# Kernel tuning notes

Hardware: AMD Instinct MI355X
Metric: run time of the kernel (lower is better)

Reference implementation:

```python
import jax, jax.numpy as jnp
import numpy as np

N, SD, VD, LD = 8192, 512, 4096, 768
TAU = 0.5
K = 6    # topk over stru->mm similarity
K2 = 6   # topk2 over mm->mm similarity
BN_EPS = 1e-5
LRELU_SLOPE = 0.01


def _mlp_bn(x, W1, b1, W2, b2, gamma, beta):
    # Linear -> LeakyReLU -> Linear -> BatchNorm1d (training mode, batch stats)
    h = x @ W1 + b1
    h = jnp.where(h >= 0, h, LRELU_SLOPE * h)
    h = h @ W2 + b2
    mu = h.mean(axis=0)
    var = h.var(axis=0)  # biased variance, as torch BN uses for normalization
    return (h - mu) / jnp.sqrt(var + BN_EPS) * gamma + beta


def _cossim(x, y):
    xn = x / (jnp.linalg.norm(x, axis=-1, keepdims=True) + 1e-12)
    yn = y / (jnp.linalg.norm(y, axis=-1, keepdims=True) + 1e-12)
    return xn @ yn.T


def _neibor_mnce_v2(stru, mm):
    sm = jnp.exp(_cossim(stru, mm) / TAU)   # [N, N]
    mmd = _cossim(mm, mm)                    # [N, N]
    _, maxSM = jax.lax.top_k(sm, K)          # [N, K]
    rows = jnp.arange(stru.shape[0])[:, None]
    pos = []
    for i in range(K):  # fixed small loop over topk columns (as in original)
        idx = maxSM[:, i]                         # [N]
        _, mm_idx = jax.lax.top_k(mmd[idx], K2)   # gather rows then topk -> [N, K2]
        pos.append(sm[rows, mm_idx])              # [N, K2]
    pos = jnp.concatenate(pos, axis=-1)           # [N, K*K2]
    return jnp.mean(-jnp.log(pos.sum(-1) / sm.sum(-1)))


def setup_inputs() -> dict:
    key = jax.random.key(0)
    ks = jax.random.split(key, 11)
    d = {
        'stru_feats': jax.random.normal(ks[0], (N, SD), jnp.float32),
        'visu_feats': jax.random.normal(ks[1], (N, VD), jnp.float32),
        'ling_feats': jax.random.normal(ks[2], (N, LD), jnp.float32),
        # fusion_l_vl params
        'Wl1': jax.random.normal(ks[3], (LD, SD), jnp.float32) / np.sqrt(LD),
        'bl1': jnp.zeros((SD,), jnp.float32),
        'Wl2': jax.random.normal(ks[4], (SD, SD), jnp.float32) / np.sqrt(SD),
        'bl2': jnp.zeros((SD,), jnp.float32),
        'gl': jnp.ones((SD,), jnp.float32),
        'betal': jnp.zeros((SD,), jnp.float32),
        # fusion_v_vl params
        'Wv1': jax.random.normal(ks[5], (VD, SD), jnp.float32) / np.sqrt(VD),
        'bv1': jnp.zeros((SD,), jnp.float32),
        'Wv2': jax.random.normal(ks[6], (SD, SD), jnp.float32) / np.sqrt(SD),
        'bv2': jnp.zeros((SD,), jnp.float32),
        'gv': jnp.ones((SD,), jnp.float32),
        'betav': jnp.zeros((SD,), jnp.float32),
    }
    return d


def reference(stru_feats, visu_feats, ling_feats,
              Wl1, bl1, Wl2, bl2, gl, betal,
              Wv1, bv1, Wv2, bv2, gv, betav):
    ling = _mlp_bn(ling_feats, Wl1, bl1, Wl2, bl2, gl, betal)
    visu = _mlp_bn(visu_feats, Wv1, bv1, Wv2, bv2, gv, betav)
    loss_sl = _neibor_mnce_v2(stru_feats, ling)
    loss_sv = _neibor_mnce_v2(stru_feats, visu)
    return (loss_sl + loss_sv, ling, visu)
```

## Files before the change

kernel.cpp:

```cpp
#include <hip/hip_runtime.h>
#include <hip/hip_bf16.h>
#include <math.h>

typedef __bf16 bf16;
typedef __attribute__((ext_vector_type(8))) __bf16 bf16x8;
typedef __attribute__((ext_vector_type(4))) float floatx4;

static_assert(sizeof(bf16x8) == 16, "bf16x8 must be 16B");

__global__ void row_normalize_kernel(const float* __restrict__ x, bf16* __restrict__ out) {
  __shared__ float red[256];
  int row = blockIdx.x;
  int t = threadIdx.x;
  float v0 = x[(size_t)row * 512 + t];
  float v1 = x[(size_t)row * 512 + t + 256];
  red[t] = v0 * v0 + v1 * v1;
  __syncthreads();
  for (int d = 128; d > 0; d >>= 1) {
    if (t < d) red[t] += red[t + d];
    __syncthreads();
  }
  float scale = 1.0f / (sqrtf(red[0]) + 1e-12f);
  out[(size_t)row * 512 + t] = (bf16)(v0 * scale);
  out[(size_t)row * 512 + t + 256] = (bf16)(v1 * scale);
}

__global__ void transpose_cast_kernel(const float* __restrict__ W, bf16* __restrict__ Wt, int K) {
  int k0 = blockIdx.x * 64;
  int n0 = blockIdx.y * 64;
  for (int i = threadIdx.x; i < 64 * 64; i += 256) {
    int kk = i & 63, nn = i >> 6;
    Wt[(size_t)(n0 + nn) * K + (k0 + kk)] = (bf16)W[(size_t)(k0 + kk) * 512 + (n0 + nn)];
  }
}

__global__ void bn_stats_kernel(const float* __restrict__ h, float* __restrict__ colsum,
                                float* __restrict__ colsumsq) {
  int col = threadIdx.x;
  int r0 = blockIdx.x * 32;
  float s = 0.f, s2 = 0.f;
  for (int r = r0; r < r0 + 32; ++r) {
    float v = h[(size_t)r * 512 + col];
    s += v;
    s2 += v * v;
  }
  atomicAdd(&colsum[col], s);
  atomicAdd(&colsumsq[col], s2);
}

__global__ void bn_apply_kernel(const float* __restrict__ h, const float* __restrict__ colsum,
                                const float* __restrict__ colsumsq, const float* __restrict__ gamma,
                                const float* __restrict__ beta, float* __restrict__ mm_out,
                                bf16* __restrict__ mmn) {
  __shared__ float red[512];
  int row = blockIdx.x, col = threadIdx.x;
  float mean = colsum[col] * (1.0f / 8192.0f);
  float var = colsumsq[col] * (1.0f / 8192.0f) - mean * mean;
  float inv = rsqrtf(var + 1e-5f);
  float y = (h[(size_t)row * 512 + col] - mean) * inv * gamma[col] + beta[col];
  mm_out[(size_t)row * 512 + col] = y;
  red[col] = y * y;
  __syncthreads();
  for (int d = 256; d > 0; d >>= 1) {
    if (col < d) red[col] += red[col + d];
    __syncthreads();
  }
  float scale = 1.0f / (sqrtf(red[0]) + 1e-12f);
  mmn[(size_t)row * 512 + col] = (bf16)(y * scale);
}

template <int MODE, bool AF32>
__launch_bounds__(256, 2) __global__
void gemm_nt_kernel(const void* __restrict__ Av, const bf16* __restrict__ B,
                    const float* __restrict__ bias, bf16* __restrict__ out_bf,
                    float* __restrict__ out_f, int K) {
  __shared__ __align__(16) bf16 As[64][72];
  __shared__ __align__(16) bf16 Bs[64][72];

  const int tid = threadIdx.x;
  const int lane = tid & 63;
  const int wave = tid >> 6;
  const int q = lane >> 4;
  const int ml = lane & 15;
  const int row0 = blockIdx.x * 64;
  const int col0 = blockIdx.y * 64;

  const float* Af = (const float*)Av;
  const bf16* Ab = (const bf16*)Av;

  floatx4 acc[4];
#pragma unroll
  for (int f = 0; f < 4; ++f) acc[f] = (floatx4)0.0f;

  for (int kt = 0; kt < K; kt += 64) {
    __syncthreads();
    for (int i = tid; i < 512; i += 256) {
      int r = i >> 3, c = (i & 7) << 3;
      if constexpr (AF32) {
        const float* p = Af + (size_t)(row0 + r) * K + kt + c;
        bf16x8 v;
#pragma unroll
        for (int e = 0; e < 8; ++e) v[e] = (bf16)p[e];
        *(bf16x8*)&As[r][c] = v;
      } else {
        *(bf16x8*)&As[r][c] = *(const bf16x8*)(Ab + (size_t)(row0 + r) * K + kt + c);
      }
      *(bf16x8*)&Bs[r][c] = *(const bf16x8*)(B + (size_t)(col0 + r) * K + kt + c);
    }
    __syncthreads();
#pragma unroll
    for (int kk = 0; kk < 64; kk += 32) {
      bf16x8 a = *(const bf16x8*)&As[wave * 16 + ml][kk + q * 8];
#pragma unroll
      for (int f = 0; f < 4; ++f) {
        bf16x8 b = *(const bf16x8*)&Bs[f * 16 + ml][kk + q * 8];
        acc[f] = __builtin_amdgcn_mfma_f32_16x16x32_bf16(a, b, acc[f], 0, 0, 0);
      }
    }
  }

#pragma unroll
  for (int f = 0; f < 4; ++f) {
    int colg = col0 + f * 16 + ml;
    float bv = bias[colg];
#pragma unroll
    for (int i = 0; i < 4; ++i) {
      int rowg = row0 + wave * 16 + q * 4 + i;
      float v = acc[f][i] + bv;
      if constexpr (MODE == 0) {
        v = v >= 0.f ? v : 0.01f * v;
        out_bf[(size_t)rowg * 512 + colg] = (bf16)v;
      } else {
        out_f[(size_t)rowg * 512 + colg] = v;
      }
    }
  }
}

__device__ __forceinline__ unsigned pack_key(float v, int col) {
  unsigned u = __float_as_uint(v);
  u = (u & 0x80000000u) ? ~u : (u | 0x80000000u);
  return (u & 0xFFFFE000u) | (unsigned)(8191 - col);
}

template <bool DO_SM>
__launch_bounds__(256, 2) __global__
void topk_sm_kernel(const bf16* __restrict__ A, const bf16* __restrict__ B,
                    unsigned* __restrict__ part_keys, float* __restrict__ rowsum_part) {
  __shared__ __align__(16) bf16 Bs[2][64][128];

  const int tid = threadIdx.x;
  const int lane = tid & 63;
  const int wave = tid >> 6;
  const int q = lane >> 4;
  const int ml = lane & 15;
  const int row0 = blockIdx.x * 128;
  const int part = blockIdx.y;

  const int str = tid >> 4;
  const int scu = tid & 15;
  const int ssc = scu ^ str;

  bf16x8 afr[2][16];
#pragma unroll
  for (int g = 0; g < 2; ++g) {
    const bf16* ap = A + (size_t)(row0 + wave * 32 + g * 16 + ml) * 512 + q * 8;
#pragma unroll
    for (int s = 0; s < 16; ++s) afr[g][s] = *(const bf16x8*)(ap + s * 32);
  }

  unsigned p6[2][4][6];
#pragma unroll
  for (int g = 0; g < 2; ++g)
#pragma unroll
    for (int i = 0; i < 4; ++i)
#pragma unroll
      for (int j = 0; j < 6; ++j) p6[g][i][j] = 0u;
  float srow[2][4] = {{0.f, 0.f, 0.f, 0.f}, {0.f, 0.f, 0.f, 0.f}};

  int buf = 0;
  {
    const bf16* bp = B + (size_t)(part * 1024 + str) * 512 + scu * 8;
#pragma unroll
    for (int m = 0; m < 4; ++m)
      *(bf16x8*)&Bs[0][str + m * 16][ssc * 8] = *(const bf16x8*)(bp + (size_t)m * 16 * 512);
  }

  for (int ct = 0; ct < 16; ++ct) {
    const int col0 = part * 1024 + ct * 64;
    floatx4 acc[2][4];
#pragma unroll
    for (int g = 0; g < 2; ++g)
#pragma unroll
      for (int f = 0; f < 4; ++f) acc[g][f] = (floatx4)0.0f;

#pragma unroll
    for (int kt4 = 0; kt4 < 4; ++kt4) {
      __syncthreads();
      bf16x8 st[4];
      const bool has_next = !(ct == 15 && kt4 == 3);
      if (has_next) {
        const int nct = (kt4 == 3) ? ct + 1 : ct;
        const int nk = (kt4 == 3) ? 0 : (kt4 + 1) * 128;
        const bf16* bp = B + (size_t)(part * 1024 + nct * 64 + str) * 512 + nk + scu * 8;
#pragma unroll
        for (int m = 0; m < 4; ++m) st[m] = *(const bf16x8*)(bp + (size_t)m * 16 * 512);
      }
#pragma unroll
      for (int kk2 = 0; kk2 < 4; ++kk2) {
#pragma unroll
        for (int f = 0; f < 4; ++f) {
          const int sc2 = (kk2 * 4 + q) ^ ml;
          bf16x8 b = *(const bf16x8*)&Bs[buf][f * 16 + ml][sc2 * 8];
          acc[0][f] = __builtin_amdgcn_mfma_f32_16x16x32_bf16(afr[0][kt4 * 4 + kk2], b, acc[0][f], 0, 0, 0);
          acc[1][f] = __builtin_amdgcn_mfma_f32_16x16x32_bf16(afr[1][kt4 * 4 + kk2], b, acc[1][f], 0, 0, 0);
        }
      }
      if (has_next) {
#pragma unroll
        for (int m = 0; m < 4; ++m)
          *(bf16x8*)&Bs[buf ^ 1][str + m * 16][ssc * 8] = st[m];
      }
      buf ^= 1;
    }

#pragma unroll
    for (int g = 0; g < 2; ++g)
#pragma unroll
      for (int i = 0; i < 4; ++i) {
        if constexpr (DO_SM) {
          float s = 0.f;
#pragma unroll
          for (int f = 0; f < 4; ++f) s += __expf(2.0f * acc[g][f][i]);
          srow[g][i] += s;
        }
#pragma unroll
        for (int f = 0; f < 4; ++f) {
          unsigned key = pack_key(acc[g][f][i], col0 + f * 16 + ml);
          if (key > p6[g][i][5]) {
#pragma unroll
            for (int j = 5; j >= 1; --j) {
              bool ap = key > p6[g][i][j - 1];
              unsigned keep = (key > p6[g][i][j]) ? key : p6[g][i][j];
              p6[g][i][j] = ap ? p6[g][i][j - 1] : keep;
            }
            if (key > p6[g][i][0]) p6[g][i][0] = key;
          }
        }
      }
  }

#pragma unroll
  for (int g = 0; g < 2; ++g)
#pragma unroll
    for (int i = 0; i < 4; ++i) {
      const int lrow = wave * 32 + g * 16 + q * 4 + i;
      if constexpr (DO_SM) {
        float s = srow[g][i];
        s += __shfl_xor(s, 1);
        s += __shfl_xor(s, 2);
        s += __shfl_xor(s, 4);
        s += __shfl_xor(s, 8);
        if (ml == 0) rowsum_part[(size_t)(row0 + lrow) * 8 + part] = s;
      }
      const size_t o = ((size_t)(row0 + lrow) * 8 + part) * 6;
#pragma unroll
      for (int k = 0; k < 6; ++k) {
        unsigned mk = p6[g][i][0];
#pragma unroll
        for (int d = 1; d < 16; d <<= 1) {
          unsigned ok = (unsigned)__shfl_xor((int)mk, d);
          if (ok > mk) mk = ok;
        }
        if (ml == 0) part_keys[o + k] = mk;
        if (p6[g][i][0] == mk) {
#pragma unroll
          for (int j = 0; j < 5; ++j) p6[g][i][j] = p6[g][i][j + 1];
          p6[g][i][5] = 0u;
        }
      }
    }
}

__global__ void merge_top6_kernel(const unsigned* __restrict__ part_keys,
                                  int* __restrict__ out_idx,
                                  const float* __restrict__ rowsum_part, float* __restrict__ rowsum,
                                  int do_rowsum) {
  int row = blockIdx.x * blockDim.x + threadIdx.x;
  if (row >= 8192) return;
  unsigned best[6] = {0u, 0u, 0u, 0u, 0u, 0u};
  for (int p = 0; p < 8; ++p) {
#pragma unroll
    for (int c = 0; c < 6; ++c) {
      unsigned k = part_keys[((size_t)row * 8 + p) * 6 + c];
      if (k > best[5]) {
#pragma unroll
        for (int j = 5; j >= 1; --j) {
          bool ap = k > best[j - 1];
          unsigned keep = (k > best[j]) ? k : best[j];
          best[j] = ap ? best[j - 1] : keep;
        }
        if (k > best[0]) best[0] = k;
      }
    }
  }
#pragma unroll
  for (int j = 0; j < 6; ++j) out_idx[row * 6 + j] = 8191 - (int)(best[j] & 0x1FFFu);
  if (do_rowsum) {
    float s = 0.f;
    for (int p = 0; p < 8; ++p) s += rowsum_part[(size_t)row * 8 + p];
    rowsum[row] = s;
  }
}

__global__ void loss_kernel(const bf16* __restrict__ strun, const bf16* __restrict__ mmn,
                            const int* __restrict__ top6, const int* __restrict__ nbr,
                            const float* __restrict__ rowsum, float* __restrict__ out0) {
  int w = (int)((blockIdx.x * blockDim.x + threadIdx.x) >> 6);
  int lane = threadIdx.x & 63;
  if (w >= 8192) return;
  bf16x8 sv = *(const bf16x8*)(strun + (size_t)w * 512 + lane * 8);
  float sf[8];
#pragma unroll
  for (int e = 0; e < 8; ++e) sf[e] = (float)sv[e];
  float pos = 0.f;
  for (int k = 0; k < 6; ++k) {
    int j = top6[w * 6 + k];
#pragma unroll
    for (int l = 0; l < 6; ++l) {
      int m = nbr[j * 6 + l];
      bf16x8 mv = *(const bf16x8*)(mmn + (size_t)m * 512 + lane * 8);
      float d = 0.f;
#pragma unroll
      for (int e = 0; e < 8; ++e) d += sf[e] * (float)mv[e];
      d += __shfl_xor(d, 1);
      d += __shfl_xor(d, 2);
      d += __shfl_xor(d, 4);
      d += __shfl_xor(d, 8);
      d += __shfl_xor(d, 16);
      d += __shfl_xor(d, 32);
      pos += __expf(2.0f * d);
    }
  }
  if (lane == 0) {
    float loss_r = logf(rowsum[w]) - logf(pos);
    atomicAdd(out0, loss_r * (1.0f / 8192.0f));
  }
}

extern "C" void kernel_launch(void* const* d_in, const int* in_sizes, int n_in, void* d_out,
                              int out_size, void* d_ws, size_t ws_size, hipStream_t stream) {
  const float* stru = (const float*)d_in[0];
  const float* visu = (const float*)d_in[1];
  const float* ling = (const float*)d_in[2];
  const float* Wl1 = (const float*)d_in[3];
  const float* bl1 = (const float*)d_in[4];
  const float* Wl2 = (const float*)d_in[5];
  const float* bl2 = (const float*)d_in[6];
  const float* gl = (const float*)d_in[7];
  const float* betal = (const float*)d_in[8];
  const float* Wv1 = (const float*)d_in[9];
  const float* bv1 = (const float*)d_in[10];
  const float* Wv2 = (const float*)d_in[11];
  const float* bv2 = (const float*)d_in[12];
  const float* gv = (const float*)d_in[13];
  const float* betav = (const float*)d_in[14];
  float* out = (float*)d_out;

  char* p = (char*)d_ws;
  auto alloc = [&](size_t bytes) {
    char* r = p;
    p += (bytes + 255) & ~(size_t)255;
    return r;
  };
  bf16* strun = (bf16*)alloc((size_t)8192 * 512 * 2);
  bf16* W1t = (bf16*)alloc((size_t)512 * 4096 * 2);
  bf16* W2t = (bf16*)alloc((size_t)512 * 512 * 2);
  bf16* H1 = (bf16*)alloc((size_t)8192 * 512 * 2);
  float* H2 = (float*)alloc((size_t)8192 * 512 * 4);
  bf16* mmn = (bf16*)alloc((size_t)8192 * 512 * 2);
  float* colsum = (float*)alloc(512 * 4);
  float* colsumsq = (float*)alloc(512 * 4);
  float* rowsum_part = (float*)alloc((size_t)8192 * 8 * 4);
  float* rowsum = (float*)alloc((size_t)8192 * 4);
  unsigned* part_keys = (unsigned*)alloc((size_t)8192 * 8 * 6 * 4);
  int* nbr = (int*)alloc((size_t)8192 * 6 * 4);
  int* top6 = (int*)alloc((size_t)8192 * 6 * 4);

  hipMemsetAsync(d_out, 0, 4, stream);
  row_normalize_kernel<<<8192, 256, 0, stream>>>(stru, strun);

  for (int br = 0; br < 2; ++br) {
    const float* X = (br == 0) ? ling : visu;
    int Kin = (br == 0) ? 768 : 4096;
    const float* W1 = (br == 0) ? Wl1 : Wv1;
    const float* b1 = (br == 0) ? bl1 : bv1;
    const float* W2 = (br == 0) ? Wl2 : Wv2;
    const float* b2 = (br == 0) ? bl2 : bv2;
    const float* g = (br == 0) ? gl : gv;
    const float* bet = (br == 0) ? betal : betav;
    float* mm_out = out + 1 + (size_t)br * 8192 * 512;

    transpose_cast_kernel<<<dim3(Kin / 64, 8), 256, 0, stream>>>(W1, W1t, Kin);
    transpose_cast_kernel<<<dim3(8, 8), 256, 0, stream>>>(W2, W2t, 512);

    gemm_nt_kernel<0, true><<<dim3(128, 8), 256, 0, stream>>>(
        X, W1t, b1, H1, nullptr, Kin);
    gemm_nt_kernel<1, false><<<dim3(128, 8), 256, 0, stream>>>(
        H1, W2t, b2, nullptr, H2, 512);

    hipMemsetAsync(colsum, 0, 512 * 4, stream);
    hipMemsetAsync(colsumsq, 0, 512 * 4, stream);
    bn_stats_kernel<<<256, 512, 0, stream>>>(H2, colsum, colsumsq);
    bn_apply_kernel<<<8192, 512, 0, stream>>>(H2, colsum, colsumsq, g, bet, mm_out, mmn);

    topk_sm_kernel<false><<<dim3(64, 8), 256, 0, stream>>>(
        mmn, mmn, part_keys, nullptr);
    merge_top6_kernel<<<32, 256, 0, stream>>>(part_keys, nbr, nullptr, nullptr, 0);

    topk_sm_kernel<true><<<dim3(64, 8), 256, 0, stream>>>(
        strun, mmn, part_keys, rowsum_part);
    merge_top6_kernel<<<32, 256, 0, stream>>>(part_keys, top6, rowsum_part, rowsum, 1);

    loss_kernel<<<2048, 256, 0, stream>>>(strun, mmn, top6, nbr, rowsum, out);
  }
}
```

Baseline: 1.187 ms.

## Double-buffer GEMM with larger tiles, coalesce transpose, split top-k into more parts

```diff
diff --git a/kernel.cpp b/kernel.cpp
--- a/kernel.cpp
+++ b/kernel.cpp
@@ -26,11 +26,21 @@
 }
 
 __global__ void transpose_cast_kernel(const float* __restrict__ W, bf16* __restrict__ Wt, int K) {
+  __shared__ float t[64][65];
   int k0 = blockIdx.x * 64;
   int n0 = blockIdx.y * 64;
-  for (int i = threadIdx.x; i < 64 * 64; i += 256) {
-    int kk = i & 63, nn = i >> 6;
-    Wt[(size_t)(n0 + nn) * K + (k0 + kk)] = (bf16)W[(size_t)(k0 + kk) * 512 + (n0 + nn)];
+#pragma unroll
+  for (int m = 0; m < 16; ++m) {
+    int kk = (threadIdx.x >> 6) + m * 4;
+    int nn = threadIdx.x & 63;
+    t[kk][nn] = W[(size_t)(k0 + kk) * 512 + n0 + nn];
+  }
+  __syncthreads();
+#pragma unroll
+  for (int m = 0; m < 16; ++m) {
+    int nn = (threadIdx.x >> 6) + m * 4;
+    int kk = threadIdx.x & 63;
+    Wt[(size_t)(n0 + nn) * K + k0 + kk] = (bf16)t[kk][nn];
   }
 }
 
@@ -74,49 +84,107 @@
 void gemm_nt_kernel(const void* __restrict__ Av, const bf16* __restrict__ B,
                     const float* __restrict__ bias, bf16* __restrict__ out_bf,
                     float* __restrict__ out_f, int K) {
-  __shared__ __align__(16) bf16 As[64][72];
-  __shared__ __align__(16) bf16 Bs[64][72];
+  __shared__ __align__(16) bf16 As[2][128][64];
+  __shared__ __align__(16) bf16 Bs[2][64][64];
 
   const int tid = threadIdx.x;
   const int lane = tid & 63;
   const int wave = tid >> 6;
   const int q = lane >> 4;
   const int ml = lane & 15;
-  const int row0 = blockIdx.x * 64;
+  const int row0 = blockIdx.x * 128;
   const int col0 = blockIdx.y * 64;
 
   const float* Af = (const float*)Av;
   const bf16* Ab = (const bf16*)Av;
 
-  floatx4 acc[4];
-#pragma unroll
-  for (int f = 0; f < 4; ++f) acc[f] = (floatx4)0.0f;
-
-  for (int kt = 0; kt < K; kt += 64) {
+  const int sr = tid >> 3;
+  const int sc = tid & 7;
+
+  floatx4 acc[2][4];
+#pragma unroll
+  for (int g = 0; g < 2; ++g)
+#pragma unroll
+    for (int f = 0; f < 4; ++f) acc[g][f] = (floatx4)0.0f;
+
+  {
+#pragma unroll
+    for (int m = 0; m < 4; ++m) {
+      int r = sr + m * 32;
+      bf16x8 v;
+      if constexpr (AF32) {
+        const float* p = Af + (size_t)(row0 + r) * K + sc * 8;
+#pragma unroll
+        for (int e = 0; e < 8; ++e) v[e] = (bf16)p[e];
+      } else {
+        v = *(const bf16x8*)(Ab + (size_t)(row0 + r) * K + sc * 8);
+      }
+      *(bf16x8*)&As[0][r][(sc ^ (r & 7)) * 8] = v;
+    }
+#pragma unroll
+    for (int m = 0; m < 2; ++m) {
+      int r = sr + m * 32;
+      *(bf16x8*)&Bs[0][r][(sc ^ (r & 7)) * 8] =
+          *(const bf16x8*)(B + (size_t)(col0 + r) * K + sc * 8);
+    }
+  }
+
+  const int nsteps = K >> 6;
+  int buf = 0;
+  for (int s = 0; s < nsteps; ++s) {
     __syncthreads();
-    for (int i = tid; i < 512; i += 256) {
-      int r = i >> 3, c = (i & 7) << 3;
-      if constexpr (AF32) {
-        const float* p = Af + (size_t)(row0 + r) * K + kt + c;
+    const bool has_next = (s + 1) < nsteps;
+    floatx4 af[4][2];
+    bf16x8 ab[4];
+    bf16x8 bb[2];
+    if (has_next) {
+      const int kt = (s + 1) << 6;
+#pragma unroll
+      for (int m = 0; m < 4; ++m) {
+        if constexpr (AF32) {
+          const floatx4* p = (const floatx4*)(Af + (size_t)(row0 + sr + m * 32) * K + kt + sc * 8);
+          af[m][0] = p[0];
+          af[m][1] = p[1];
+        } else {
+          ab[m] = *(const bf16x8*)(Ab + (size_t)(row0 + sr + m * 32) * K + kt + sc * 8);
+        }
+      }
+#pragma unroll
+      for (int m = 0; m < 2; ++m)
+        bb[m] = *(const bf16x8*)(B + (size_t)(col0 + sr + m * 32) * K + kt + sc * 8);
+    }
+#pragma unroll
+    for (int kh = 0; kh < 2; ++kh) {
+      const int slot = ((q + kh * 4) ^ (ml & 7)) * 8;
+      bf16x8 a0 = *(const bf16x8*)&As[buf][wave * 32 + ml][slot];
+      bf16x8 a1 = *(const bf16x8*)&As[buf][wave * 32 + 16 + ml][slot];
+#pragma unroll
+      for (int f = 0; f < 4; ++f) {
+        bf16x8 b = *(const bf16x8*)&Bs[buf][f * 16 + ml][slot];
+        acc[0][f] = __builtin_amdgcn_mfma_f32_16x16x32_bf16(a0, b, acc[0][f], 0, 0, 0);
+        acc[1][f] = __builtin_amdgcn_mfma_f32_16x16x32_bf16(a1, b, acc[1][f], 0, 0, 0);
+      }
+    }
+    if (has_next) {
+#pragma unroll
+      for (int m = 0; m < 4; ++m) {
+        int r = sr + m * 32;
         bf16x8 v;
-#pragma unroll
-        for (int e = 0; e < 8; ++e) v[e] = (bf16)p[e];
-        *(bf16x8*)&As[r][c] = v;
-      } else {
-        *(bf16x8*)&As[r][c] = *(const bf16x8*)(Ab + (size_t)(row0 + r) * K + kt + c);
-      }
-      *(bf16x8*)&Bs[r][c] = *(const bf16x8*)(B + (size_t)(col0 + r) * K + kt + c);
-    }
-    __syncthreads();
-#pragma unroll
-    for (int kk = 0; kk < 64; kk += 32) {
-      bf16x8 a = *(const bf16x8*)&As[wave * 16 + ml][kk + q * 8];
-#pragma unroll
-      for (int f = 0; f < 4; ++f) {
-        bf16x8 b = *(const bf16x8*)&Bs[f * 16 + ml][kk + q * 8];
-        acc[f] = __builtin_amdgcn_mfma_f32_16x16x32_bf16(a, b, acc[f], 0, 0, 0);
-      }
-    }
+        if constexpr (AF32) {
+#pragma unroll
+          for (int e = 0; e < 8; ++e) v[e] = (bf16)af[m][e >> 2][e & 3];
+        } else {
+          v = ab[m];
+        }
+        *(bf16x8*)&As[buf ^ 1][r][(sc ^ (r & 7)) * 8] = v;
+      }
+#pragma unroll
+      for (int m = 0; m < 2; ++m) {
+        int r = sr + m * 32;
+        *(bf16x8*)&Bs[buf ^ 1][r][(sc ^ (r & 7)) * 8] = bb[m];
+      }
+    }
+    buf ^= 1;
   }
 
 #pragma unroll
@@ -124,16 +192,18 @@
     int colg = col0 + f * 16 + ml;
     float bv = bias[colg];
 #pragma unroll
-    for (int i = 0; i < 4; ++i) {
-      int rowg = row0 + wave * 16 + q * 4 + i;
-      float v = acc[f][i] + bv;
-      if constexpr (MODE == 0) {
-        v = v >= 0.f ? v : 0.01f * v;
-        out_bf[(size_t)rowg * 512 + colg] = (bf16)v;
-      } else {
-        out_f[(size_t)rowg * 512 + colg] = v;
-      }
-    }
+    for (int g = 0; g < 2; ++g)
+#pragma unroll
+      for (int i = 0; i < 4; ++i) {
+        int rowg = row0 + wave * 32 + g * 16 + q * 4 + i;
+        float v = acc[g][f][i] + bv;
+        if constexpr (MODE == 0) {
+          v = v >= 0.f ? v : 0.01f * v;
+          out_bf[(size_t)rowg * 512 + colg] = (bf16)v;
+        } else {
+          out_f[(size_t)rowg * 512 + colg] = v;
+        }
+      }
   }
 }
 
@@ -142,6 +212,8 @@
   u = (u & 0x80000000u) ? ~u : (u | 0x80000000u);
   return (u & 0xFFFFE000u) | (unsigned)(8191 - col);
 }
+
+#define NPARTS 16
 
 template <bool DO_SM>
 __launch_bounds__(256, 2) __global__
@@ -180,14 +252,14 @@
 
   int buf = 0;
   {
-    const bf16* bp = B + (size_t)(part * 1024 + str) * 512 + scu * 8;
+    const bf16* bp = B + (size_t)(part * 512 + str) * 512 + scu * 8;
 #pragma unroll
     for (int m = 0; m < 4; ++m)
       *(bf16x8*)&Bs[0][str + m * 16][ssc * 8] = *(const bf16x8*)(bp + (size_t)m * 16 * 512);
   }
 
-  for (int ct = 0; ct < 16; ++ct) {
-    const int col0 = part * 1024 + ct * 64;
+  for (int ct = 0; ct < 8; ++ct) {
+    const int col0 = part * 512 + ct * 64;
     floatx4 acc[2][4];
 #pragma unroll
     for (int g = 0; g < 2; ++g)
@@ -198,11 +270,11 @@
     for (int kt4 = 0; kt4 < 4; ++kt4) {
       __syncthreads();
       bf16x8 st[4];
-      const bool has_next = !(ct == 15 && kt4 == 3);
+      const bool has_next = !(ct == 7 && kt4 == 3);
       if (has_next) {
         const int nct = (kt4 == 3) ? ct + 1 : ct;
         const int nk = (kt4 == 3) ? 0 : (kt4 + 1) * 128;
-        const bf16* bp = B + (size_t)(part * 1024 + nct * 64 + str) * 512 + nk + scu * 8;
+        const bf16* bp = B + (size_t)(part * 512 + nct * 64 + str) * 512 + nk + scu * 8;
 #pragma unroll
         for (int m = 0; m < 4; ++m) st[m] = *(const bf16x8*)(bp + (size_t)m * 16 * 512);
       }
@@ -261,9 +333,9 @@
         s += __shfl_xor(s, 2);
         s += __shfl_xor(s, 4);
         s += __shfl_xor(s, 8);
-        if (ml == 0) rowsum_part[(size_t)(row0 + lrow) * 8 + part] = s;
-      }
-      const size_t o = ((size_t)(row0 + lrow) * 8 + part) * 6;
+        if (ml == 0) rowsum_part[(size_t)(row0 + lrow) * NPARTS + part] = s;
+      }
+      const size_t o = ((size_t)(row0 + lrow) * NPARTS + part) * 6;
 #pragma unroll
       for (int k = 0; k < 6; ++k) {
         unsigned mk = p6[g][i][0];
@@ -289,10 +361,10 @@
   int row = blockIdx.x * blockDim.x + threadIdx.x;
   if (row >= 8192) return;
   unsigned best[6] = {0u, 0u, 0u, 0u, 0u, 0u};
-  for (int p = 0; p < 8; ++p) {
+  for (int p = 0; p < NPARTS; ++p) {
 #pragma unroll
     for (int c = 0; c < 6; ++c) {
-      unsigned k = part_keys[((size_t)row * 8 + p) * 6 + c];
+      unsigned k = part_keys[((size_t)row * NPARTS + p) * 6 + c];
       if (k > best[5]) {
 #pragma unroll
         for (int j = 5; j >= 1; --j) {
@@ -308,7 +380,7 @@
   for (int j = 0; j < 6; ++j) out_idx[row * 6 + j] = 8191 - (int)(best[j] & 0x1FFFu);
   if (do_rowsum) {
     float s = 0.f;
-    for (int p = 0; p < 8; ++p) s += rowsum_part[(size_t)row * 8 + p];
+    for (int p = 0; p < NPARTS; ++p) s += rowsum_part[(size_t)row * NPARTS + p];
     rowsum[row] = s;
   }
 }
@@ -381,9 +453,9 @@
   bf16* mmn = (bf16*)alloc((size_t)8192 * 512 * 2);
   float* colsum = (float*)alloc(512 * 4);
   float* colsumsq = (float*)alloc(512 * 4);
-  float* rowsum_part = (float*)alloc((size_t)8192 * 8 * 4);
+  float* rowsum_part = (float*)alloc((size_t)8192 * NPARTS * 4);
   float* rowsum = (float*)alloc((size_t)8192 * 4);
-  unsigned* part_keys = (unsigned*)alloc((size_t)8192 * 8 * 6 * 4);
+  unsigned* part_keys = (unsigned*)alloc((size_t)8192 * NPARTS * 6 * 4);
   int* nbr = (int*)alloc((size_t)8192 * 6 * 4);
   int* top6 = (int*)alloc((size_t)8192 * 6 * 4);
 
@@ -404,9 +476,9 @@
     transpose_cast_kernel<<<dim3(Kin / 64, 8), 256, 0, stream>>>(W1, W1t, Kin);
     transpose_cast_kernel<<<dim3(8, 8), 256, 0, stream>>>(W2, W2t, 512);
 
-    gemm_nt_kernel<0, true><<<dim3(128, 8), 256, 0, stream>>>(
+    gemm_nt_kernel<0, true><<<dim3(64, 8), 256, 0, stream>>>(
         X, W1t, b1, H1, nullptr, Kin);
-    gemm_nt_kernel<1, false><<<dim3(128, 8), 256, 0, stream>>>(
+    gemm_nt_kernel<1, false><<<dim3(64, 8), 256, 0, stream>>>(
         H1, W2t, b2, nullptr, H2, 512);
 
     hipMemsetAsync(colsum, 0, 512 * 4, stream);
@@ -414,11 +486,11 @@
     bn_stats_kernel<<<256, 512, 0, stream>>>(H2, colsum, colsumsq);
     bn_apply_kernel<<<8192, 512, 0, stream>>>(H2, colsum, colsumsq, g, bet, mm_out, mmn);
 
-    topk_sm_kernel<false><<<dim3(64, 8), 256, 0, stream>>>(
+    topk_sm_kernel<false><<<dim3(64, NPARTS), 256, 0, stream>>>(
         mmn, mmn, part_keys, nullptr);
     merge_top6_kernel<<<32, 256, 0, stream>>>(part_keys, nbr, nullptr, nullptr, 0);
 
-    topk_sm_kernel<true><<<dim3(64, 8), 256, 0, stream>>>(
+    topk_sm_kernel<true><<<dim3(64, NPARTS), 256, 0, stream>>>(
         strun, mmn, part_keys, rowsum_part);
     merge_top6_kernel<<<32, 256, 0, stream>>>(part_keys, top6, rowsum_part, rowsum, 1);
 
```

After: 1.202 ms. Within noise of the previous version (+1.3%).
